# Performance work log

Measured on AMD Instinct MI355X. Metric: run time of the kernel, lower is better.

## Reference

```python
import jax, jax.numpy as jnp
import numpy as np

B, C_IN, C_OUT, N, K = 4, 64, 128, 81920, 10


def setup_inputs() -> dict:
    key = jax.random.key(0)
    k1, k2, k3, k4 = jax.random.split(key, 4)
    x = jax.random.normal(k1, (B, C_IN, N), dtype=jnp.float32)
    indices = jax.random.randint(k2, (N, K), 0, N, dtype=jnp.int64)
    # Conv2d(in, out, kernel=(1,K)) weight [C_out, C_in, 1, K] -> store as [C_out, C_in, K]
    fan_in = C_IN * K
    bound = 1.0 / np.sqrt(fan_in)
    W = jax.random.uniform(k3, (C_OUT, C_IN, K), jnp.float32, -bound, bound)
    b = jax.random.uniform(k4, (C_OUT,), jnp.float32, -bound, bound)
    return {"input": x, "indices": indices, "W": W, "b": b}


def reference(input, indices, W, b):
    # gather neighbor pixels: [B, C_in, N, K]
    col = input[:, :, indices]
    # 1xK conv == contraction over (C_in, K): [B, C_out, N]
    out = jnp.einsum('bcnk,ock->bon', col, W) + b[None, :, None]
    return out
```

## Files before the change

kernel.cpp:

```cpp
#include <hip/hip_runtime.h>
#include <hip/hip_bf16.h>
#include <stdint.h>

#define NPTS 81920
#define CIN  64
#define COUT 128
#define BATCH 4
#define KNB  10
#define NT   32

typedef __attribute__((ext_vector_type(8)))  short bf16x8;
typedef __attribute__((ext_vector_type(16))) float f32x16;

static __device__ __forceinline__ unsigned short f2bf(float f) {
    unsigned int u = __float_as_uint(f);
    u += 0x7fffu + ((u >> 16) & 1u);
    return (unsigned short)(u >> 16);
}

static __device__ __forceinline__ void gload16(const void* g, void* l) {
    __builtin_amdgcn_global_load_lds(
        (const __attribute__((address_space(1))) unsigned int*)g,
        (__attribute__((address_space(3))) unsigned int*)l, 16, 0, 0);
}

__global__ __launch_bounds__(256) void k_transpose(const float* __restrict__ x,
                                                   unsigned short* __restrict__ xT) {
    const int m = blockIdx.x * 256 + threadIdx.x;
    const int b = blockIdx.y;
    const float* xb = x + (size_t)b * CIN * NPTS + m;

    unsigned int v[CIN / 2];
    #pragma unroll
    for (int i = 0; i < CIN / 2; ++i) {
        float f0 = __builtin_nontemporal_load(&xb[(size_t)(2 * i) * NPTS]);
        float f1 = __builtin_nontemporal_load(&xb[(size_t)(2 * i + 1) * NPTS]);
        v[i] = (unsigned int)f2bf(f0) | ((unsigned int)f2bf(f1) << 16);
    }
    uint4* dst = (uint4*)(xT + ((size_t)m * BATCH + b) * CIN);
    #pragma unroll
    for (int i = 0; i < 8; ++i) {
        uint4 w; w.x = v[4*i]; w.y = v[4*i+1]; w.z = v[4*i+2]; w.w = v[4*i+3];
        dst[i] = w;
    }
}

__global__ __launch_bounds__(256) void k_wconv(const float* __restrict__ W,
                                               unsigned short* __restrict__ Wb) {
    const int e  = blockIdx.x * 256 + threadIdx.x;
    const int j  = e & 7;
    const int l  = (e >> 3) & 63;
    const int f  = (e >> 9) & 3;
    const int sg = e >> 11;
    const int o  = 32 * f + (l & 31);
    const int ck = sg * 16 + 8 * (l >> 5) + j;
    const int kn = ck >> 6;
    const int c  = ck & 63;
    Wb[e] = f2bf(W[(o * CIN + c) * KNB + kn]);
}

__global__ __launch_bounds__(512, 4) void k_main(const unsigned short* __restrict__ xT,
                                                 const unsigned short* __restrict__ Wb,
                                                 const float* __restrict__ bias,
                                                 const int* __restrict__ idx,
                                                 float* __restrict__ out) {
    __shared__ char smem[2][NT * 512];

    const int t    = threadIdx.x;
    const int lane = t & 63;
    const int wv   = t >> 6;
    const int op   = wv & 1;
    const int b    = wv >> 1;
    const int hw   = lane >> 5;
    const int l31  = lane & 31;
    const int nb   = blockIdx.x * NT;

    const char* xb = (const char*)xT;
    const bf16x8* wbase = (const bf16x8*)Wb;

    int soff[KNB][2];
    #pragma unroll
    for (int k = 0; k < KNB; ++k) {
        #pragma unroll
        for (int i = 0; i < 2; ++i) {
            const int row = (wv << 2) + (i << 1) + hw;
            const int r   = idx[(nb + row) * KNB + k];
            soff[k][i] = r * 512 + ((l31 ^ (row & 7)) << 4);
        }
    }

    f32x16 acc[2];
    #pragma unroll
    for (int p = 0; p < 2; ++p)
        #pragma unroll
        for (int r = 0; r < 16; ++r) acc[p][r] = 0.f;

    #define STAGE(kk, buf)                                                      \
        {                                                                       \
            _Pragma("unroll")                                                   \
            for (int i = 0; i < 2; ++i) {                                       \
                gload16(xb + soff[kk][i],                                       \
                        &smem[buf][(((wv << 2) + (i << 1))) << 9]);             \
            }                                                                   \
        }

    STAGE(0, 0);
    __syncthreads();

    #pragma unroll
    for (int k = 0; k < KNB; ++k) {
        if (k + 1 < KNB) STAGE(k + 1, (k + 1) & 1);

        bf16x8 a[2][4];
        #pragma unroll
        for (int p = 0; p < 2; ++p)
            #pragma unroll
            for (int ks = 0; ks < 4; ++ks)
                a[p][ks] = wbase[((k * 4 + ks) * 4 + (op * 2 + p)) * 64 + lane];

        const char* sb = smem[k & 1];
        #pragma unroll
        for (int ks = 0; ks < 4; ++ks) {
            const int g    = b * 8 + ks * 2 + hw;
            const int byte = (g ^ (l31 & 7)) << 4;
            const bf16x8 bf = *(const bf16x8*)(sb + l31 * 512 + byte);
            #pragma unroll
            for (int p = 0; p < 2; ++p)
                acc[p] = __builtin_amdgcn_mfma_f32_32x32x16_bf16(
                    a[p][ks], bf, acc[p], 0, 0, 0);
        }
        __syncthreads();
    }
    #undef STAGE

    const int n = nb + l31;
    #pragma unroll
    for (int p = 0; p < 2; ++p) {
        #pragma unroll
        for (int r = 0; r < 16; ++r) {
            const int o = 32 * (op * 2 + p) + (r & 3) + 8 * (r >> 2) + 4 * hw;
            const float v = acc[p][r] + bias[o];
            __builtin_nontemporal_store(v, &out[(size_t)(b * COUT + o) * NPTS + n]);
        }
    }
}

extern "C" void kernel_launch(void* const* d_in, const int* in_sizes, int n_in,
                              void* d_out, int out_size, void* d_ws, size_t ws_size,
                              hipStream_t stream) {
    const float* x    = (const float*)d_in[0];
    const int*   idx  = (const int*)d_in[1];
    const float* W    = (const float*)d_in[2];
    const float* bias = (const float*)d_in[3];
    float* out = (float*)d_out;

    unsigned short* xT = (unsigned short*)d_ws;
    unsigned short* Wb = (unsigned short*)((char*)d_ws + (size_t)BATCH * NPTS * CIN * 2);

    k_transpose<<<dim3(NPTS / 256, BATCH), 256, 0, stream>>>(x, xT);
    k_wconv<<<dim3((COUT * KNB * CIN) / 256), 256, 0, stream>>>(W, Wb);
    k_main<<<dim3(NPTS / NT), 512, 0, stream>>>(xT, Wb, bias, idx, out);
}
```

Measured before the change: 145.2 us.

## Halve block waves, double per-wave batch work, and triple-buffer gathered neighbor rows

```diff
diff --git a/kernel.cpp b/kernel.cpp
--- a/kernel.cpp
+++ b/kernel.cpp
@@ -59,18 +59,18 @@
     Wb[e] = f2bf(W[(o * CIN + c) * KNB + kn]);
 }
 
-__global__ __launch_bounds__(512, 4) void k_main(const unsigned short* __restrict__ xT,
+__global__ __launch_bounds__(256, 3) void k_main(const unsigned short* __restrict__ xT,
                                                  const unsigned short* __restrict__ Wb,
                                                  const float* __restrict__ bias,
                                                  const int* __restrict__ idx,
                                                  float* __restrict__ out) {
-    __shared__ char smem[2][NT * 512];
+    __shared__ char smem[3][NT * 512];
 
     const int t    = threadIdx.x;
     const int lane = t & 63;
     const int wv   = t >> 6;
     const int op   = wv & 1;
-    const int b    = wv >> 1;
+    const int bq   = wv >> 1;
     const int hw   = lane >> 5;
     const int l31  = lane & 31;
     const int nb   = blockIdx.x * NT;
@@ -78,38 +78,44 @@
     const char* xb = (const char*)xT;
     const bf16x8* wbase = (const bf16x8*)Wb;
 
-    int soff[KNB][2];
+    int soff[KNB][4];
     #pragma unroll
     for (int k = 0; k < KNB; ++k) {
         #pragma unroll
-        for (int i = 0; i < 2; ++i) {
-            const int row = (wv << 2) + (i << 1) + hw;
+        for (int i = 0; i < 4; ++i) {
+            const int row = (wv << 3) + (i << 1) + hw;
             const int r   = idx[(nb + row) * KNB + k];
             soff[k][i] = r * 512 + ((l31 ^ (row & 7)) << 4);
         }
     }
 
-    f32x16 acc[2];
+    f32x16 acc[2][2];
     #pragma unroll
     for (int p = 0; p < 2; ++p)
         #pragma unroll
-        for (int r = 0; r < 16; ++r) acc[p][r] = 0.f;
+        for (int bb = 0; bb < 2; ++bb)
+            #pragma unroll
+            for (int r = 0; r < 16; ++r) acc[p][bb][r] = 0.f;
 
     #define STAGE(kk, buf)                                                      \
         {                                                                       \
             _Pragma("unroll")                                                   \
-            for (int i = 0; i < 2; ++i) {                                       \
+            for (int i = 0; i < 4; ++i) {                                       \
                 gload16(xb + soff[kk][i],                                       \
-                        &smem[buf][(((wv << 2) + (i << 1))) << 9]);             \
+                        &smem[buf][((wv << 3) + (i << 1)) << 9]);               \
             }                                                                   \
         }
 
     STAGE(0, 0);
-    __syncthreads();
+    STAGE(1, 1);
 
     #pragma unroll
     for (int k = 0; k < KNB; ++k) {
-        if (k + 1 < KNB) STAGE(k + 1, (k + 1) & 1);
+        if (k == KNB - 1) asm volatile("s_waitcnt vmcnt(0)" ::: "memory");
+        else              asm volatile("s_waitcnt vmcnt(4)" ::: "memory");
+        __builtin_amdgcn_s_barrier();
+
+        if (k + 2 < KNB) STAGE(k + 2, (k + 2) % 3);
 
         bf16x8 a[2][4];
         #pragma unroll
@@ -118,18 +124,23 @@
             for (int ks = 0; ks < 4; ++ks)
                 a[p][ks] = wbase[((k * 4 + ks) * 4 + (op * 2 + p)) * 64 + lane];
 
-        const char* sb = smem[k & 1];
+        const char* sb = smem[k % 3];
         #pragma unroll
         for (int ks = 0; ks < 4; ++ks) {
-            const int g    = b * 8 + ks * 2 + hw;
-            const int byte = (g ^ (l31 & 7)) << 4;
-            const bf16x8 bf = *(const bf16x8*)(sb + l31 * 512 + byte);
+            bf16x8 bf[2];
+            #pragma unroll
+            for (int bb = 0; bb < 2; ++bb) {
+                const int g    = (bq * 2 + bb) * 8 + ks * 2 + hw;
+                const int byte = (g ^ (l31 & 7)) << 4;
+                bf[bb] = *(const bf16x8*)(sb + l31 * 512 + byte);
+            }
             #pragma unroll
             for (int p = 0; p < 2; ++p)
-                acc[p] = __builtin_amdgcn_mfma_f32_32x32x16_bf16(
-                    a[p][ks], bf, acc[p], 0, 0, 0);
+                #pragma unroll
+                for (int bb = 0; bb < 2; ++bb)
+                    acc[p][bb] = __builtin_amdgcn_mfma_f32_32x32x16_bf16(
+                        a[p][ks], bf[bb], acc[p][bb], 0, 0, 0);
         }
-        __syncthreads();
     }
     #undef STAGE
 
@@ -137,10 +148,14 @@
     #pragma unroll
     for (int p = 0; p < 2; ++p) {
         #pragma unroll
-        for (int r = 0; r < 16; ++r) {
-            const int o = 32 * (op * 2 + p) + (r & 3) + 8 * (r >> 2) + 4 * hw;
-            const float v = acc[p][r] + bias[o];
-            __builtin_nontemporal_store(v, &out[(size_t)(b * COUT + o) * NPTS + n]);
+        for (int bb = 0; bb < 2; ++bb) {
+            const int b = bq * 2 + bb;
+            #pragma unroll
+            for (int r = 0; r < 16; ++r) {
+                const int o = 32 * (op * 2 + p) + (r & 3) + 8 * (r >> 2) + 4 * hw;
+                const float v = acc[p][bb][r] + bias[o];
+                __builtin_nontemporal_store(v, &out[(size_t)(b * COUT + o) * NPTS + n]);
+            }
         }
     }
 }
@@ -159,5 +174,5 @@
 
     k_transpose<<<dim3(NPTS / 256, BATCH), 256, 0, stream>>>(x, xT);
     k_wconv<<<dim3((COUT * KNB * CIN) / 256), 256, 0, stream>>>(W, Wb);
-    k_main<<<dim3(NPTS / NT), 512, 0, stream>>>(xT, Wb, bias, idx, out);
+    k_main<<<dim3(NPTS / NT), 256, 0, stream>>>(xT, Wb, bias, idx, out);
 }
```

Measured after the change: 135.3 us. 6.8% less time.

## Register-staged gather with transposed LDS layout and weight prefetch in main kernel

Applied to the files above, without the earlier changes.

```diff
diff --git a/kernel.cpp b/kernel.cpp
--- a/kernel.cpp
+++ b/kernel.cpp
@@ -16,12 +16,6 @@
     unsigned int u = __float_as_uint(f);
     u += 0x7fffu + ((u >> 16) & 1u);
     return (unsigned short)(u >> 16);
-}
-
-static __device__ __forceinline__ void gload16(const void* g, void* l) {
-    __builtin_amdgcn_global_load_lds(
-        (const __attribute__((address_space(1))) unsigned int*)g,
-        (__attribute__((address_space(3))) unsigned int*)l, 16, 0, 0);
 }
 
 __global__ __launch_bounds__(256) void k_transpose(const float* __restrict__ x,
@@ -69,8 +63,8 @@
     const int t    = threadIdx.x;
     const int lane = t & 63;
     const int wv   = t >> 6;
-    const int op   = wv & 1;
-    const int b    = wv >> 1;
+    const int op   = wv & 3;
+    const int bq   = wv >> 2;
     const int hw   = lane >> 5;
     const int l31  = lane & 31;
     const int nb   = blockIdx.x * NT;
@@ -78,68 +72,78 @@
     const char* xb = (const char*)xT;
     const bf16x8* wbase = (const bf16x8*)Wb;
 
+    const int row0 = (wv << 2) + hw;
+    const int row1 = row0 + 2;
     int soff[KNB][2];
     #pragma unroll
     for (int k = 0; k < KNB; ++k) {
-        #pragma unroll
-        for (int i = 0; i < 2; ++i) {
-            const int row = (wv << 2) + (i << 1) + hw;
-            const int r   = idx[(nb + row) * KNB + k];
-            soff[k][i] = r * 512 + ((l31 ^ (row & 7)) << 4);
-        }
+        soff[k][0] = idx[(nb + row0) * KNB + k] * 512;
+        soff[k][1] = idx[(nb + row1) * KNB + k] * 512;
     }
+    const int wo0 = (l31 << 9) + (((row0 ^ l31) & 31) << 4);
+    const int wo1 = (l31 << 9) + (((row1 ^ l31) & 31) << 4);
 
     f32x16 acc[2];
     #pragma unroll
-    for (int p = 0; p < 2; ++p)
+    for (int bb = 0; bb < 2; ++bb)
         #pragma unroll
-        for (int r = 0; r < 16; ++r) acc[p][r] = 0.f;
+        for (int r = 0; r < 16; ++r) acc[bb][r] = 0.f;
 
-    #define STAGE(kk, buf)                                                      \
-        {                                                                       \
-            _Pragma("unroll")                                                   \
-            for (int i = 0; i < 2; ++i) {                                       \
-                gload16(xb + soff[kk][i],                                       \
-                        &smem[buf][(((wv << 2) + (i << 1))) << 9]);             \
-            }                                                                   \
-        }
+    uint4 b0 = *(const uint4*)(xb + soff[0][0] + l31 * 16);
+    uint4 b1 = *(const uint4*)(xb + soff[0][1] + l31 * 16);
+    asm volatile("s_waitcnt vmcnt(0)" ::: "memory");
+    *(uint4*)(smem[0] + wo0) = b0;
+    *(uint4*)(smem[0] + wo1) = b1;
 
-    STAGE(0, 0);
-    __syncthreads();
+    bf16x8 a[4], an[4];
+    #pragma unroll
+    for (int ks = 0; ks < 4; ++ks)
+        a[ks] = wbase[((0 * 4 + ks) * 4 + op) * 64 + lane];
+    uint4 bn0 = *(const uint4*)(xb + soff[1][0] + l31 * 16);
+    uint4 bn1 = *(const uint4*)(xb + soff[1][1] + l31 * 16);
 
     #pragma unroll
     for (int k = 0; k < KNB; ++k) {
-        if (k + 1 < KNB) STAGE(k + 1, (k + 1) & 1);
+        asm volatile("s_waitcnt vmcnt(0) lgkmcnt(0)" ::: "memory");
+        __builtin_amdgcn_s_barrier();
 
-        bf16x8 a[2][4];
-        #pragma unroll
-        for (int p = 0; p < 2; ++p)
+        if (k + 1 < KNB) {
+            char* d = smem[(k + 1) & 1];
+            *(uint4*)(d + wo0) = bn0;
+            *(uint4*)(d + wo1) = bn1;
             #pragma unroll
             for (int ks = 0; ks < 4; ++ks)
-                a[p][ks] = wbase[((k * 4 + ks) * 4 + (op * 2 + p)) * 64 + lane];
+                an[ks] = wbase[(((k + 1) * 4 + ks) * 4 + op) * 64 + lane];
+        }
+        if (k + 2 < KNB) {
+            bn0 = *(const uint4*)(xb + soff[k + 2][0] + l31 * 16);
+            bn1 = *(const uint4*)(xb + soff[k + 2][1] + l31 * 16);
+        }
 
         const char* sb = smem[k & 1];
         #pragma unroll
         for (int ks = 0; ks < 4; ++ks) {
-            const int g    = b * 8 + ks * 2 + hw;
-            const int byte = (g ^ (l31 & 7)) << 4;
-            const bf16x8 bf = *(const bf16x8*)(sb + l31 * 512 + byte);
             #pragma unroll
-            for (int p = 0; p < 2; ++p)
-                acc[p] = __builtin_amdgcn_mfma_f32_32x32x16_bf16(
-                    a[p][ks], bf, acc[p], 0, 0, 0);
+            for (int bb = 0; bb < 2; ++bb) {
+                const int g = (bq * 2 + bb) * 8 + ks * 2 + hw;
+                const bf16x8 bf =
+                    *(const bf16x8*)(sb + (g << 9) + (((l31 ^ g) & 31) << 4));
+                acc[bb] = __builtin_amdgcn_mfma_f32_32x32x16_bf16(
+                    a[ks], bf, acc[bb], 0, 0, 0);
+            }
         }
-        __syncthreads();
+        #pragma unroll
+        for (int ks = 0; ks < 4; ++ks) a[ks] = an[ks];
     }
-    #undef STAGE
 
     const int n = nb + l31;
     #pragma unroll
-    for (int p = 0; p < 2; ++p) {
+    for (int bb = 0; bb < 2; ++bb) {
+        const int b = bq * 2 + bb;
         #pragma unroll
         for (int r = 0; r < 16; ++r) {
-            const int o = 32 * (op * 2 + p) + (r & 3) + 8 * (r >> 2) + 4 * hw;
-            const float v = acc[p][r] + bias[o];
+            const int o = 32 * op + (r & 3) + 8 * (r >> 2) + 4 * hw;
+            const float v = acc[bb][r] + bias[o];
             __builtin_nontemporal_store(v, &out[(size_t)(b * COUT + o) * NPTS + n]);
         }
     }
```

After: 133.9 us. 1.08x faster.
